# Kernel tuning notes

Measured on AMD Instinct MI355X. Metric: run time of the kernel, lower is better.

Reference implementation:

```python
import jax, jax.numpy as jnp
import numpy as np


def xnorm(x, g):
    # x * gamma / ||x||_2 along last dim (no eps, matching torch.norm)
    n = jnp.sqrt(jnp.sum(x * x, axis=-1, keepdims=True))
    return x * g / n


def setup_inputs() -> dict:
    key = jax.random.key(0)
    ks = jax.random.split(key, 6)
    B, N, D = 8, 8192, 512
    H, DK, DV = 8, 64, 64
    std = 0.001
    return {
        "queries": jax.random.normal(ks[0], (B, N, D), dtype=jnp.float32),
        # weights stored [in, out] (transposed vs torch Linear)
        "Wq": jax.random.normal(ks[1], (D, H * DK), dtype=jnp.float32) * std,
        "bq": jnp.zeros((H * DK,), dtype=jnp.float32),
        "Wk": jax.random.normal(ks[2], (D, H * DK), dtype=jnp.float32) * std,
        "bk": jnp.zeros((H * DK,), dtype=jnp.float32),
        "Wv": jax.random.normal(ks[3], (D, H * DV), dtype=jnp.float32) * std,
        "bv": jnp.zeros((H * DV,), dtype=jnp.float32),
        "Wo": jax.random.normal(ks[4], (H * DV, D), dtype=jnp.float32) * std,
        "bo": jnp.zeros((D,), dtype=jnp.float32),
        "gamma": jax.random.normal(ks[5], (1, H, 1, 1), dtype=jnp.float32),
    }


def reference(queries, Wq, bq, Wk, bk, Wv, bv, Wo, bo, gamma):
    B, N, D = queries.shape
    H, DK = 8, 64
    DV = 64
    q = (queries @ Wq + bq).reshape(B, N, H, DK)  # bnhd
    k = (queries @ Wk + bk).reshape(B, N, H, DK)
    v = (queries @ Wv + bv).reshape(B, N, H, DV)
    # kv = k^T @ v per (batch, head): [B,H,DK,DV]
    kv = jnp.einsum("bnhk,bnhv->bhkv", k, v)
    kv_n = xnorm(kv, gamma)                       # norm over DV axis
    q_n = xnorm(q.transpose(0, 2, 1, 3), gamma)   # bhnd, norm over DK axis
    out = jnp.einsum("bhnk,bhkv->bnhv", q_n, kv_n).reshape(B, N, H * DV)
    return out @ Wo + bo
```

## Files before the change

### kernel.cpp

```cpp
#include <hip/hip_runtime.h>

typedef __attribute__((ext_vector_type(8))) short s8v;
typedef __attribute__((ext_vector_type(4))) float f4v;

__device__ __forceinline__ unsigned short f2bf(float f) {
  unsigned int u = __float_as_uint(f);
  u += 0x7FFFu + ((u >> 16) & 1u);
  return (unsigned short)(u >> 16);
}
__device__ __forceinline__ float bf2f(unsigned short s) {
  return __uint_as_float(((unsigned int)s) << 16);
}

__device__ __forceinline__ void gld16(const void* g, void* l) {
  __builtin_amdgcn_global_load_lds(
      (const __attribute__((address_space(1))) unsigned int*)g,
      (__attribute__((address_space(3))) unsigned int*)l, 16, 0, 0);
}

#define TILE_SYNC() asm volatile("s_waitcnt vmcnt(0) lgkmcnt(0)\n\ts_barrier" ::: "memory")

__global__ __launch_bounds__(256)
void convert_x_kernel(const float* __restrict__ X, unsigned short* __restrict__ Xbf)
{
  size_t base = ((size_t)blockIdx.x * 256 + threadIdx.x) * 8;
  float4 a = *(const float4*)&X[base];
  float4 b = *(const float4*)&X[base + 4];
  s8v p = (s8v){ (short)f2bf(a.x), (short)f2bf(a.y), (short)f2bf(a.z), (short)f2bf(a.w),
                 (short)f2bf(b.x), (short)f2bf(b.y), (short)f2bf(b.z), (short)f2bf(b.w) };
  *(s8v*)&Xbf[base] = p;
}

__global__ __launch_bounds__(256)
void transpose_w_kernel(const float* __restrict__ Wq, const float* __restrict__ Wk,
                        const float* __restrict__ Wv, unsigned short* __restrict__ Wt)
{
  __shared__ float T[64][68];
  const int kt = blockIdx.x, nt = blockIdx.y;
  const float* W = (nt < 8) ? Wq : (nt < 16 ? Wk : Wv);
  const int n0 = (nt & 7) * 64, k0 = kt * 64;
  const int t = threadIdx.x;
  #pragma unroll
  for (int it = 0; it < 4; ++it) {
    int idx = it * 256 + t;
    int k = idx >> 4, n4 = (idx & 15) << 2;
    *(float4*)&T[k][n4] = *(const float4*)&W[(size_t)(k0 + k) * 512 + n0 + n4];
  }
  __syncthreads();
  #pragma unroll
  for (int it = 0; it < 2; ++it) {
    int idx = it * 256 + t;
    int n = idx >> 3, k8 = (idx & 7) << 3;
    s8v p;
    #pragma unroll
    for (int j = 0; j < 8; ++j) p[j] = (short)f2bf(T[k8 + j][n]);
    *(s8v*)&Wt[((size_t)nt * 64 + n) * 512 + k0 + k8] = p;
  }
}

__global__ __launch_bounds__(256, 2)
void gemm_qkv_kernel(const unsigned short* __restrict__ Xbf,
                     const unsigned short* __restrict__ Wt,
                     const float* __restrict__ bq, const float* __restrict__ bk,
                     const float* __restrict__ bv,
                     const float* __restrict__ gamma,
                     unsigned short* __restrict__ qhat,
                     unsigned short* __restrict__ kvT)
{
  __shared__ short As[8192];
  __shared__ short Bs[8192];
  const int t = threadIdx.x;
  const int nb = blockIdx.x, rb = blockIdx.y;
  const int wave = t >> 6, lane = t & 63;
  const int wm = wave & 1, wn = wave >> 1;
  const int quad = lane >> 4, l16 = lane & 15;
  const int row0 = rb * 128;
  const int ncol0 = nb * 128;

  const unsigned short* ap[4];
  const unsigned short* bp[4];
  #pragma unroll
  for (int i = 0; i < 4; ++i) {
    int s = i * 256 + t;
    int m = s >> 3;
    int kb = (s & 7) ^ (m & 7);
    ap[i] = Xbf + (size_t)(row0 + m) * 512 + kb * 8;
    bp[i] = Wt + (size_t)(ncol0 + m) * 512 + kb * 8;
  }

  f4v acc[4][4];
  #pragma unroll
  for (int i = 0; i < 4; ++i)
    #pragma unroll
    for (int j = 0; j < 4; ++j) acc[i][j] = (f4v){0.f, 0.f, 0.f, 0.f};

  for (int kt = 0; kt < 512; kt += 64) {
    __syncthreads();
    #pragma unroll
    for (int i = 0; i < 4; ++i) {
      int s8 = (i * 256 + t) * 8;
      gld16(ap[i] + kt, &As[s8]);
      gld16(bp[i] + kt, &Bs[s8]);
    }
    __syncthreads();
    #pragma unroll
    for (int ks = 0; ks < 2; ++ks) {
      s8v a[4], b[4];
      #pragma unroll
      for (int mi = 0; mi < 4; ++mi) {
        int r = wm * 64 + mi * 16 + l16;
        int slot = r * 8 + ((ks * 4 + quad) ^ (r & 7));
        a[mi] = *(const s8v*)&As[slot * 8];
      }
      #pragma unroll
      for (int nj = 0; nj < 4; ++nj) {
        int r = wn * 64 + nj * 16 + l16;
        int slot = r * 8 + ((ks * 4 + quad) ^ (r & 7));
        b[nj] = *(const s8v*)&Bs[slot * 8];
      }
      #pragma unroll
      for (int mi = 0; mi < 4; ++mi)
        #pragma unroll
        for (int nj = 0; nj < 4; ++nj)
          acc[mi][nj] = __builtin_amdgcn_mfma_f32_16x16x32_bf16(a[mi], b[nj], acc[mi][nj], 0, 0, 0);
    }
  }

  if (nb < 4) {
    #pragma unroll
    for (int nj = 0; nj < 4; ++nj) {
      int colg = ncol0 + wn * 64 + nj * 16 + l16;
      float bias = bq[colg];
      #pragma unroll
      for (int mi = 0; mi < 4; ++mi) {
        acc[mi][nj][0] += bias; acc[mi][nj][1] += bias;
        acc[mi][nj][2] += bias; acc[mi][nj][3] += bias;
      }
    }
    float g = gamma[nb * 2 + wn];
    #pragma unroll
    for (int mi = 0; mi < 4; ++mi)
      #pragma unroll
      for (int rr = 0; rr < 4; ++rr) {
        float ss = acc[mi][0][rr] * acc[mi][0][rr] + acc[mi][1][rr] * acc[mi][1][rr]
                 + acc[mi][2][rr] * acc[mi][2][rr] + acc[mi][3][rr] * acc[mi][3][rr];
        ss += __shfl_xor(ss, 1);
        ss += __shfl_xor(ss, 2);
        ss += __shfl_xor(ss, 4);
        ss += __shfl_xor(ss, 8);
        float scale = g * rsqrtf(ss);
        acc[mi][0][rr] *= scale; acc[mi][1][rr] *= scale;
        acc[mi][2][rr] *= scale; acc[mi][3][rr] *= scale;
      }
    const int colbase = ncol0 + wn * 64;
    #pragma unroll
    for (int mi = 0; mi < 4; ++mi)
      #pragma unroll
      for (int nj = 0; nj < 4; ++nj)
        #pragma unroll
        for (int rr = 0; rr < 4; ++rr) {
          int row = row0 + wm * 64 + mi * 16 + quad * 4 + rr;
          int col = colbase + nj * 16 + l16;
          qhat[(size_t)row * 512 + col] = f2bf(acc[mi][nj][rr]);
        }
  } else {
    const int sect = (nb - 4) >> 2;
    const float* bb = sect ? bv : bk;
    const int bidx = row0 >> 13;
    const int nb4 = (nb - 4) & 3;
    const int nrow = (row0 & 8191) + wm * 64 + quad * 4;
    #pragma unroll
    for (int nj = 0; nj < 4; ++nj) {
      int cis = nb4 * 128 + wn * 64 + nj * 16 + l16;
      float bias = bb[cis];
      int h = cis >> 6, dk = cis & 63;
      unsigned short* rowp = kvT + (size_t)((sect * 64 + bidx * 8 + h) * 64 + dk) * 8192;
      #pragma unroll
      for (int mi = 0; mi < 4; ++mi) {
        unsigned int lo = (unsigned int)f2bf(acc[mi][nj][0] + bias)
                        | ((unsigned int)f2bf(acc[mi][nj][1] + bias) << 16);
        unsigned int hi = (unsigned int)f2bf(acc[mi][nj][2] + bias)
                        | ((unsigned int)f2bf(acc[mi][nj][3] + bias) << 16);
        uint2 pk; pk.x = lo; pk.y = hi;
        *(uint2*)&rowp[nrow + mi * 16] = pk;
      }
    }
  }
}

__global__ __launch_bounds__(256)
void kv_accum_kernel(const unsigned short* __restrict__ kvT, float* __restrict__ kvpart)
{
  const int t = threadIdx.x;
  const int bh = blockIdx.x, chunk = blockIdx.y;
  const int wave = t >> 6, lane = t & 63;
  const int quad = lane >> 4, l16 = lane & 15;
  const unsigned short* kb_ = kvT + (size_t)bh * 64 * 8192;
  const unsigned short* vb_ = kvT + (size_t)(64 + bh) * 64 * 8192;
  const int n0 = chunk * 512 + wave * 128 + quad * 8;

  f4v acc[4][4];
  #pragma unroll
  for (int i = 0; i < 4; ++i)
    #pragma unroll
    for (int j = 0; j < 4; ++j) acc[i][j] = (f4v){0.f, 0.f, 0.f, 0.f};

  s8v a0[4], b0[4], a1[4], b1[4];
  #pragma unroll
  for (int mi = 0; mi < 4; ++mi) {
    a0[mi] = *(const s8v*)&kb_[(size_t)(mi * 16 + l16) * 8192 + n0];
    b0[mi] = *(const s8v*)&vb_[(size_t)(mi * 16 + l16) * 8192 + n0];
  }

#define KV_STEP(AC, BC, AN, BN, S)                                             \
  {                                                                            \
    if ((S) < 3) {                                                             \
      int nn = n0 + ((S) + 1) * 32;                                            \
      _Pragma("unroll")                                                        \
      for (int mi = 0; mi < 4; ++mi) {                                         \
        AN[mi] = *(const s8v*)&kb_[(size_t)(mi * 16 + l16) * 8192 + nn];       \
        BN[mi] = *(const s8v*)&vb_[(size_t)(mi * 16 + l16) * 8192 + nn];       \
      }                                                                        \
    }                                                                          \
    _Pragma("unroll")                                                          \
    for (int mi = 0; mi < 4; ++mi)                                             \
      _Pragma("unroll")                                                        \
      for (int nj = 0; nj < 4; ++nj)                                           \
        acc[mi][nj] = __builtin_amdgcn_mfma_f32_16x16x32_bf16(AC[mi], BC[nj],  \
                                                              acc[mi][nj], 0, 0, 0); \
  }

  KV_STEP(a0, b0, a1, b1, 0)
  KV_STEP(a1, b1, a0, b0, 1)
  KV_STEP(a0, b0, a1, b1, 2)
  KV_STEP(a1, b1, a0, b0, 3)
#undef KV_STEP

  float* dst = kvpart + ((size_t)(chunk * 4 + wave) * 64 + bh) * 4096;
  #pragma unroll
  for (int mi = 0; mi < 4; ++mi)
    #pragma unroll
    for (int nj = 0; nj < 4; ++nj)
      #pragma unroll
      for (int rr = 0; rr < 4; ++rr)
        dst[(mi * 16 + quad * 4 + rr) * 64 + nj * 16 + l16] = acc[mi][nj][rr];
}

__global__ __launch_bounds__(256)
void kv_reduce_kernel(const float* __restrict__ kvpart, float* __restrict__ kvbuf)
{
  const int bh = blockIdx.x, seg = blockIdx.y, t = threadIdx.x;
  #pragma unroll
  for (int e = 0; e < 2; ++e) {
    int i = seg * 512 + e * 256 + t;
    float s = 0.f;
    for (int c = 0; c < 64; ++c) s += kvpart[((size_t)c * 64 + bh) * 4096 + i];
    kvbuf[(size_t)bh * 4096 + i] = s;
  }
}

__global__ __launch_bounds__(256)
void build_w2t_kernel(const float* __restrict__ kvbuf, const float* __restrict__ Wo,
                      const float* __restrict__ gamma, unsigned short* __restrict__ W2t)
{
  __shared__ float WoS[512][16];
  const int b = blockIdx.x, dt = blockIdx.y;
  const int d0 = dt * 16;
  const int t = threadIdx.x;
  for (int i = 0; i < 32; ++i) {
    int flat = i * 256 + t;
    int rr_ = flat >> 4, c = flat & 15;
    WoS[rr_][c] = Wo[(size_t)rr_ * 512 + d0 + c];
  }
  __syncthreads();
  for (int rr = 0; rr < 2; ++rr) {
    int r = rr * 256 + t;
    int h = r >> 6, k = r & 63;
    const float* krow = kvbuf + ((size_t)b * 8 + h) * 4096 + (size_t)k * 64;
    float ss = 0.f;
    #pragma unroll
    for (int v = 0; v < 64; v += 4) {
      float4 x = *(const float4*)&krow[v];
      ss += x.x * x.x + x.y * x.y + x.z * x.z + x.w * x.w;
    }
    float scale = gamma[h] * rsqrtf(ss);
    f4v accv[4];
    #pragma unroll
    for (int j = 0; j < 4; ++j) accv[j] = (f4v){0.f, 0.f, 0.f, 0.f};
    for (int v = 0; v < 64; ++v) {
      float m = krow[v] * scale;
      const float* w = &WoS[h * 64 + v][0];
      #pragma unroll
      for (int j4 = 0; j4 < 4; ++j4) {
        float4 ww = *(const float4*)&w[j4 * 4];
        accv[j4][0] = fmaf(m, ww.x, accv[j4][0]);
        accv[j4][1] = fmaf(m, ww.y, accv[j4][1]);
        accv[j4][2] = fmaf(m, ww.z, accv[j4][2]);
        accv[j4][3] = fmaf(m, ww.w, accv[j4][3]);
      }
    }
    #pragma unroll
    for (int j = 0; j < 16; ++j)
      W2t[((size_t)b * 512 + d0 + j) * 512 + r] = f2bf(accv[j >> 2][j & 3]);
  }
}

__global__ __launch_bounds__(512, 2)
void gemm_out_kernel(const unsigned short* __restrict__ qhat,
                     const unsigned short* __restrict__ W2t,
                     const float* __restrict__ bo,
                     float* __restrict__ out)
{
  __shared__ short As[2][16384];
  __shared__ short Bs[2][16384];
  const int t = threadIdx.x;
  const int o = blockIdx.x;
  const int swz = (o & 7) * 64 + (o >> 3);
  const int nb = swz & 1, rb = swz >> 1;
  const int wave = t >> 6, lane = t & 63;
  const int wm = wave & 1, wn = wave >> 1;
  const int quad = lane >> 4, l16 = lane & 15;
  const int row0 = rb * 256, ncol0 = nb * 256;
  const unsigned short* Wb = W2t + (size_t)(rb >> 5) * 262144;

  const unsigned short* ap[4];
  const unsigned short* bp[4];
  int ldst[4];
  #pragma unroll
  for (int i = 0; i < 4; ++i) {
    int s = i * 512 + t;
    int m = s >> 3, kb = (s & 7) ^ (m & 7);
    ap[i] = qhat + (size_t)(row0 + m) * 512 + kb * 8;
    bp[i] = Wb + (size_t)(ncol0 + m) * 512 + kb * 8;
    ldst[i] = s * 8;
  }

  f4v acc[8][4];
  #pragma unroll
  for (int i = 0; i < 8; ++i)
    #pragma unroll
    for (int j = 0; j < 4; ++j) acc[i][j] = (f4v){0.f, 0.f, 0.f, 0.f};

  #pragma unroll
  for (int i = 0; i < 4; ++i) {
    gld16(ap[i], &As[0][ldst[i]]);
    gld16(bp[i], &Bs[0][ldst[i]]);
  }
  TILE_SYNC();

  for (int kt = 0; kt < 8; ++kt) {
    const int cur = kt & 1;
    const short* Ac = As[cur];
    const short* Bc = Bs[cur];
    short* An = (short*)As[cur ^ 1];
    short* Bn = (short*)Bs[cur ^ 1];
    const int koff = (kt + 1) * 64;
    const bool pf = kt < 7;
    s8v afr[4][2], bfr[4][2];

    if (pf) {
      gld16(ap[0] + koff, &An[ldst[0]]);
      gld16(ap[1] + koff, &An[ldst[1]]);
      gld16(bp[0] + koff, &Bn[ldst[0]]);
      gld16(bp[1] + koff, &Bn[ldst[1]]);
    }
    #pragma unroll
    for (int nj = 0; nj < 4; ++nj)
      #pragma unroll
      for (int ks = 0; ks < 2; ++ks) {
        int r = wn * 64 + nj * 16 + l16;
        bfr[nj][ks] = *(const s8v*)&Bc[(r * 8 + ((ks * 4 + quad) ^ (r & 7))) * 8];
      }
    #pragma unroll
    for (int mi = 0; mi < 4; ++mi)
      #pragma unroll
      for (int ks = 0; ks < 2; ++ks) {
        int r = wm * 128 + mi * 16 + l16;
        afr[mi][ks] = *(const s8v*)&Ac[(r * 8 + ((ks * 4 + quad) ^ (r & 7))) * 8];
      }
    __builtin_amdgcn_s_setprio(1);
    #pragma unroll
    for (int mi = 0; mi < 4; ++mi)
      #pragma unroll
      for (int nj = 0; nj < 2; ++nj)
        #pragma unroll
        for (int ks = 0; ks < 2; ++ks)
          acc[mi][nj] = __builtin_amdgcn_mfma_f32_16x16x32_bf16(afr[mi][ks], bfr[nj][ks], acc[mi][nj], 0, 0, 0);
    __builtin_amdgcn_s_setprio(0);
    __builtin_amdgcn_s_barrier();

    if (pf) {
      gld16(ap[2] + koff, &An[ldst[2]]);
      gld16(ap[3] + koff, &An[ldst[3]]);
      gld16(bp[2] + koff, &Bn[ldst[2]]);
      gld16(bp[3] + koff, &Bn[ldst[3]]);
    }
    __builtin_amdgcn_s_setprio(1);
    #pragma unroll
    for (int mi = 0; mi < 4; ++mi)
      #pragma unroll
      for (int nj = 2; nj < 4; ++nj)
        #pragma unroll
        for (int ks = 0; ks < 2; ++ks)
          acc[mi][nj] = __builtin_amdgcn_mfma_f32_16x16x32_bf16(afr[mi][ks], bfr[nj][ks], acc[mi][nj], 0, 0, 0);
    __builtin_amdgcn_s_setprio(0);
    __builtin_amdgcn_s_barrier();

    #pragma unroll
    for (int mi = 0; mi < 4; ++mi)
      #pragma unroll
      for (int ks = 0; ks < 2; ++ks) {
        int r = wm * 128 + (4 + mi) * 16 + l16;
        afr[mi][ks] = *(const s8v*)&Ac[(r * 8 + ((ks * 4 + quad) ^ (r & 7))) * 8];
      }
    __builtin_amdgcn_s_setprio(1);
    #pragma unroll
    for (int mi = 0; mi < 4; ++mi)
      #pragma unroll
      for (int nj = 0; nj < 2; ++nj)
        #pragma unroll
        for (int ks = 0; ks < 2; ++ks)
          acc[4 + mi][nj] = __builtin_amdgcn_mfma_f32_16x16x32_bf16(afr[mi][ks], bfr[nj][ks], acc[4 + mi][nj], 0, 0, 0);
    __builtin_amdgcn_s_setprio(0);
    __builtin_amdgcn_s_barrier();

    __builtin_amdgcn_s_setprio(1);
    #pragma unroll
    for (int mi = 0; mi < 4; ++mi)
      #pragma unroll
      for (int nj = 2; nj < 4; ++nj)
        #pragma unroll
        for (int ks = 0; ks < 2; ++ks)
          acc[4 + mi][nj] = __builtin_amdgcn_mfma_f32_16x16x32_bf16(afr[mi][ks], bfr[nj][ks], acc[4 + mi][nj], 0, 0, 0);
    __builtin_amdgcn_s_setprio(0);
    TILE_SYNC();
  }

  const int colbase = ncol0 + wn * 64;
  #pragma unroll
  for (int nj = 0; nj < 4; ++nj) {
    float bias = bo[colbase + nj * 16 + l16];
    #pragma unroll
    for (int mi = 0; mi < 8; ++mi)
      #pragma unroll
      for (int rr = 0; rr < 4; ++rr) {
        int row = row0 + wm * 128 + mi * 16 + quad * 4 + rr;
        int col = colbase + nj * 16 + l16;
        out[(size_t)row * 512 + col] = acc[mi][nj][rr] + bias;
      }
  }
}

extern "C" void kernel_launch(void* const* d_in, const int* in_sizes, int n_in,
                              void* d_out, int out_size, void* d_ws, size_t ws_size,
                              hipStream_t stream)
{
  (void)in_sizes; (void)n_in; (void)out_size; (void)ws_size;
  const float* X     = (const float*)d_in[0];
  const float* Wq    = (const float*)d_in[1];
  const float* bq    = (const float*)d_in[2];
  const float* Wk    = (const float*)d_in[3];
  const float* bk    = (const float*)d_in[4];
  const float* Wv    = (const float*)d_in[5];
  const float* bv    = (const float*)d_in[6];
  const float* Wo    = (const float*)d_in[7];
  const float* bo    = (const float*)d_in[8];
  const float* gamma = (const float*)d_in[9];

  char* ws = (char*)d_ws;
  unsigned short* qhat = (unsigned short*)ws;
  unsigned short* kvT  = (unsigned short*)(ws + 67108864);
  unsigned short* Xbf  = (unsigned short*)(ws + 201326592);
  float* kvpart = (float*)(ws + 201326592);
  unsigned short* Wt  = (unsigned short*)(ws + 201326592 + 67108864);
  float* kvbuf        = (float*)(ws + 201326592 + 67108864 + 1572864);
  unsigned short* W2t = (unsigned short*)(ws + 201326592 + 67108864 + 1572864 + 1048576);

  dim3 blk(256);
  convert_x_kernel<<<16384, blk, 0, stream>>>(X, Xbf);
  transpose_w_kernel<<<dim3(8, 24), blk, 0, stream>>>(Wq, Wk, Wv, Wt);
  gemm_qkv_kernel<<<dim3(12, 512), blk, 0, stream>>>(Xbf, Wt, bq, bk, bv, gamma, qhat, kvT);
  kv_accum_kernel<<<dim3(64, 16), blk, 0, stream>>>(kvT, kvpart);
  kv_reduce_kernel<<<dim3(64, 8), blk, 0, stream>>>(kvpart, kvbuf);
  build_w2t_kernel<<<dim3(8, 32), blk, 0, stream>>>(kvbuf, Wo, gamma, W2t);
  gemm_out_kernel<<<512, dim3(512), 0, stream>>>(qhat, W2t, bo, (float*)d_out);
}
```

Before: 504.8 us.

## Retile QKV GEMM to 256x256 double-buffered pipeline with grid swizzle

The QKV projection GEMM moves from 128x128 tiles with 256 threads and single-buffered LDS to 256x256 tiles with 512 threads and double-buffered LDS. Loads for the next k-tile are issued in pieces between MFMA phases, guarded by partial vmcnt waits, and a 1D grid with an XCD-aware swizzle replaces the 2D grid. The output GEMM's pipeline is restructured the same way, dropping intermediate barriers and the full wait at the end of each tile. The aim is to reuse each tile more and hide global-load latency. In exchange, LDS use and register pressure rise (128 KB of LDS per block), which can lower occupancy.

Result: slower. 516.5 us (+2.3%).

```diff
diff --git a/kernel.cpp b/kernel.cpp
--- a/kernel.cpp
+++ b/kernel.cpp
@@ -18,7 +18,11 @@
       (__attribute__((address_space(3))) unsigned int*)l, 16, 0, 0);
 }
 
-#define TILE_SYNC() asm volatile("s_waitcnt vmcnt(0) lgkmcnt(0)\n\ts_barrier" ::: "memory")
+#define WAITVM4() asm volatile("s_waitcnt vmcnt(4)" ::: "memory")
+#define WAITVM2() asm volatile("s_waitcnt vmcnt(2)" ::: "memory")
+#define WAITVM0() asm volatile("s_waitcnt vmcnt(0)" ::: "memory")
+#define WAITLGKM() asm volatile("s_waitcnt lgkmcnt(0)" ::: "memory")
+#define SBAR() asm volatile("s_barrier" ::: "memory")
 
 __global__ __launch_bounds__(256)
 void convert_x_kernel(const float* __restrict__ X, unsigned short* __restrict__ Xbf)
@@ -58,7 +62,7 @@
   }
 }
 
-__global__ __launch_bounds__(256, 2)
+__global__ __launch_bounds__(512, 2)
 void gemm_qkv_kernel(const unsigned short* __restrict__ Xbf,
                      const unsigned short* __restrict__ Wt,
                      const float* __restrict__ bq, const float* __restrict__ bk,
@@ -67,79 +71,132 @@
                      unsigned short* __restrict__ qhat,
                      unsigned short* __restrict__ kvT)
 {
-  __shared__ short As[8192];
-  __shared__ short Bs[8192];
+  __shared__ short As[2][16384];
+  __shared__ short Bs[2][16384];
   const int t = threadIdx.x;
-  const int nb = blockIdx.x, rb = blockIdx.y;
+  const int o = blockIdx.x;
+  const int swz = (o & 7) * 192 + (o >> 3);
+  const int nb = swz % 6, rb = swz / 6;
   const int wave = t >> 6, lane = t & 63;
   const int wm = wave & 1, wn = wave >> 1;
   const int quad = lane >> 4, l16 = lane & 15;
-  const int row0 = rb * 128;
-  const int ncol0 = nb * 128;
+  const int row0 = rb * 256, ncol0 = nb * 256;
 
   const unsigned short* ap[4];
   const unsigned short* bp[4];
+  int ldst[4];
   #pragma unroll
   for (int i = 0; i < 4; ++i) {
-    int s = i * 256 + t;
-    int m = s >> 3;
-    int kb = (s & 7) ^ (m & 7);
+    int s = i * 512 + t;
+    int m = s >> 3, kb = (s & 7) ^ (m & 7);
     ap[i] = Xbf + (size_t)(row0 + m) * 512 + kb * 8;
     bp[i] = Wt + (size_t)(ncol0 + m) * 512 + kb * 8;
-  }
-
-  f4v acc[4][4];
-  #pragma unroll
-  for (int i = 0; i < 4; ++i)
+    ldst[i] = s * 8;
+  }
+
+  f4v acc[8][4];
+  #pragma unroll
+  for (int i = 0; i < 8; ++i)
     #pragma unroll
     for (int j = 0; j < 4; ++j) acc[i][j] = (f4v){0.f, 0.f, 0.f, 0.f};
 
-  for (int kt = 0; kt < 512; kt += 64) {
-    __syncthreads();
-    #pragma unroll
-    for (int i = 0; i < 4; ++i) {
-      int s8 = (i * 256 + t) * 8;
-      gld16(ap[i] + kt, &As[s8]);
-      gld16(bp[i] + kt, &Bs[s8]);
-    }
-    __syncthreads();
-    #pragma unroll
-    for (int ks = 0; ks < 2; ++ks) {
-      s8v a[4], b[4];
-      #pragma unroll
-      for (int mi = 0; mi < 4; ++mi) {
-        int r = wm * 64 + mi * 16 + l16;
-        int slot = r * 8 + ((ks * 4 + quad) ^ (r & 7));
-        a[mi] = *(const s8v*)&As[slot * 8];
-      }
-      #pragma unroll
-      for (int nj = 0; nj < 4; ++nj) {
+  gld16(bp[0], &Bs[0][ldst[0]]);
+  gld16(bp[1], &Bs[0][ldst[1]]);
+  gld16(bp[2], &Bs[0][ldst[2]]);
+  gld16(bp[3], &Bs[0][ldst[3]]);
+  gld16(ap[0], &As[0][ldst[0]]);
+  gld16(ap[2], &As[0][ldst[2]]);
+  gld16(ap[1], &As[0][ldst[1]]);
+  gld16(ap[3], &As[0][ldst[3]]);
+
+  for (int kt = 0; kt < 8; ++kt) {
+    const bool pf = kt < 7;
+    const int cur = kt & 1;
+    const short* Ac = As[cur];
+    const short* Bc = Bs[cur];
+    short* An = (short*)As[cur ^ 1];
+    short* Bn = (short*)Bs[cur ^ 1];
+    const int koff = (kt + 1) * 64;
+    s8v afr[4][2], bfr[4][2];
+
+    if (pf) {
+      gld16(bp[0] + koff, &Bn[ldst[0]]);
+      gld16(bp[1] + koff, &Bn[ldst[1]]);
+    }
+    if (pf) { WAITVM4(); } else { WAITVM2(); }
+    SBAR();
+
+    #pragma unroll
+    for (int nj = 0; nj < 4; ++nj)
+      #pragma unroll
+      for (int ks = 0; ks < 2; ++ks) {
         int r = wn * 64 + nj * 16 + l16;
-        int slot = r * 8 + ((ks * 4 + quad) ^ (r & 7));
-        b[nj] = *(const s8v*)&Bs[slot * 8];
-      }
-      #pragma unroll
-      for (int mi = 0; mi < 4; ++mi)
+        bfr[nj][ks] = *(const s8v*)&Bc[(r * 8 + ((ks * 4 + quad) ^ (r & 7))) * 8];
+      }
+    #pragma unroll
+    for (int mi = 0; mi < 4; ++mi)
+      #pragma unroll
+      for (int ks = 0; ks < 2; ++ks) {
+        int r = wm * 128 + mi * 16 + l16;
+        afr[mi][ks] = *(const s8v*)&Ac[(r * 8 + ((ks * 4 + quad) ^ (r & 7))) * 8];
+      }
+    __builtin_amdgcn_s_setprio(1);
+    #pragma unroll
+    for (int mi = 0; mi < 4; ++mi)
+      #pragma unroll
+      for (int nj = 0; nj < 4; ++nj)
         #pragma unroll
-        for (int nj = 0; nj < 4; ++nj)
-          acc[mi][nj] = __builtin_amdgcn_mfma_f32_16x16x32_bf16(a[mi], b[nj], acc[mi][nj], 0, 0, 0);
-    }
-  }
-
-  if (nb < 4) {
+        for (int ks = 0; ks < 2; ++ks)
+          acc[mi][nj] = __builtin_amdgcn_mfma_f32_16x16x32_bf16(afr[mi][ks], bfr[nj][ks], acc[mi][nj], 0, 0, 0);
+    __builtin_amdgcn_s_setprio(0);
+
+    if (pf) {
+      gld16(bp[2] + koff, &Bn[ldst[2]]);
+      gld16(bp[3] + koff, &Bn[ldst[3]]);
+    }
+    if (pf) { WAITVM4(); } else { WAITVM0(); }
+    SBAR();
+
+    #pragma unroll
+    for (int mi = 0; mi < 4; ++mi)
+      #pragma unroll
+      for (int ks = 0; ks < 2; ++ks) {
+        int r = wm * 128 + 64 + mi * 16 + l16;
+        afr[mi][ks] = *(const s8v*)&Ac[(r * 8 + ((ks * 4 + quad) ^ (r & 7))) * 8];
+      }
+    if (pf) {
+      gld16(ap[0] + koff, &An[ldst[0]]);
+      gld16(ap[2] + koff, &An[ldst[2]]);
+      gld16(ap[1] + koff, &An[ldst[1]]);
+      gld16(ap[3] + koff, &An[ldst[3]]);
+    }
+    __builtin_amdgcn_s_setprio(1);
+    #pragma unroll
+    for (int mi = 0; mi < 4; ++mi)
+      #pragma unroll
+      for (int nj = 0; nj < 4; ++nj)
+        #pragma unroll
+        for (int ks = 0; ks < 2; ++ks)
+          acc[4 + mi][nj] = __builtin_amdgcn_mfma_f32_16x16x32_bf16(afr[mi][ks], bfr[nj][ks], acc[4 + mi][nj], 0, 0, 0);
+    __builtin_amdgcn_s_setprio(0);
+    WAITLGKM();
+    SBAR();
+  }
+
+  if (nb < 2) {
     #pragma unroll
     for (int nj = 0; nj < 4; ++nj) {
       int colg = ncol0 + wn * 64 + nj * 16 + l16;
       float bias = bq[colg];
       #pragma unroll
-      for (int mi = 0; mi < 4; ++mi) {
+      for (int mi = 0; mi < 8; ++mi) {
         acc[mi][nj][0] += bias; acc[mi][nj][1] += bias;
         acc[mi][nj][2] += bias; acc[mi][nj][3] += bias;
       }
     }
-    float g = gamma[nb * 2 + wn];
-    #pragma unroll
-    for (int mi = 0; mi < 4; ++mi)
+    float g = gamma[nb * 4 + wn];
+    #pragma unroll
+    for (int mi = 0; mi < 8; ++mi)
       #pragma unroll
       for (int rr = 0; rr < 4; ++rr) {
         float ss = acc[mi][0][rr] * acc[mi][0][rr] + acc[mi][1][rr] * acc[mi][1][rr]
@@ -154,29 +211,28 @@
       }
     const int colbase = ncol0 + wn * 64;
     #pragma unroll
-    for (int mi = 0; mi < 4; ++mi)
+    for (int mi = 0; mi < 8; ++mi)
       #pragma unroll
       for (int nj = 0; nj < 4; ++nj)
         #pragma unroll
         for (int rr = 0; rr < 4; ++rr) {
-          int row = row0 + wm * 64 + mi * 16 + quad * 4 + rr;
+          int row = row0 + wm * 128 + mi * 16 + quad * 4 + rr;
           int col = colbase + nj * 16 + l16;
           qhat[(size_t)row * 512 + col] = f2bf(acc[mi][nj][rr]);
         }
   } else {
-    const int sect = (nb - 4) >> 2;
+    const int sect = (nb - 2) >> 1;
     const float* bb = sect ? bv : bk;
     const int bidx = row0 >> 13;
-    const int nb4 = (nb - 4) & 3;
-    const int nrow = (row0 & 8191) + wm * 64 + quad * 4;
+    const int nrow = (row0 & 8191) + wm * 128 + quad * 4;
     #pragma unroll
     for (int nj = 0; nj < 4; ++nj) {
-      int cis = nb4 * 128 + wn * 64 + nj * 16 + l16;
+      int cis = ((nb - 2) & 1) * 256 + wn * 64 + nj * 16 + l16;
       float bias = bb[cis];
       int h = cis >> 6, dk = cis & 63;
       unsigned short* rowp = kvT + (size_t)((sect * 64 + bidx * 8 + h) * 64 + dk) * 8192;
       #pragma unroll
-      for (int mi = 0; mi < 4; ++mi) {
+      for (int mi = 0; mi < 8; ++mi) {
         unsigned int lo = (unsigned int)f2bf(acc[mi][nj][0] + bias)
                         | ((unsigned int)f2bf(acc[mi][nj][1] + bias) << 16);
         unsigned int hi = (unsigned int)f2bf(acc[mi][nj][2] + bias)
@@ -341,29 +397,32 @@
     #pragma unroll
     for (int j = 0; j < 4; ++j) acc[i][j] = (f4v){0.f, 0.f, 0.f, 0.f};
 
-  #pragma unroll
-  for (int i = 0; i < 4; ++i) {
-    gld16(ap[i], &As[0][ldst[i]]);
-    gld16(bp[i], &Bs[0][ldst[i]]);
-  }
-  TILE_SYNC();
+  gld16(bp[0], &Bs[0][ldst[0]]);
+  gld16(bp[1], &Bs[0][ldst[1]]);
+  gld16(bp[2], &Bs[0][ldst[2]]);
+  gld16(bp[3], &Bs[0][ldst[3]]);
+  gld16(ap[0], &As[0][ldst[0]]);
+  gld16(ap[2], &As[0][ldst[2]]);
+  gld16(ap[1], &As[0][ldst[1]]);
+  gld16(ap[3], &As[0][ldst[3]]);
 
   for (int kt = 0; kt < 8; ++kt) {
+    const bool pf = kt < 7;
     const int cur = kt & 1;
     const short* Ac = As[cur];
     const short* Bc = Bs[cur];
     short* An = (short*)As[cur ^ 1];
     short* Bn = (short*)Bs[cur ^ 1];
     const int koff = (kt + 1) * 64;
-    const bool pf = kt < 7;
     s8v afr[4][2], bfr[4][2];
 
     if (pf) {
-      gld16(ap[0] + koff, &An[ldst[0]]);
-      gld16(ap[1] + koff, &An[ldst[1]]);
       gld16(bp[0] + koff, &Bn[ldst[0]]);
       gld16(bp[1] + koff, &Bn[ldst[1]]);
     }
+    if (pf) { WAITVM4(); } else { WAITVM2(); }
+    SBAR();
+
     #pragma unroll
     for (int nj = 0; nj < 4; ++nj)
       #pragma unroll
@@ -382,58 +441,43 @@
     #pragma unroll
     for (int mi = 0; mi < 4; ++mi)
       #pragma unroll
-      for (int nj = 0; nj < 2; ++nj)
+      for (int nj = 0; nj < 4; ++nj)
         #pragma unroll
         for (int ks = 0; ks < 2; ++ks)
           acc[mi][nj] = __builtin_amdgcn_mfma_f32_16x16x32_bf16(afr[mi][ks], bfr[nj][ks], acc[mi][nj], 0, 0, 0);
     __builtin_amdgcn_s_setprio(0);
-    __builtin_amdgcn_s_barrier();
 
     if (pf) {
-      gld16(ap[2] + koff, &An[ldst[2]]);
-      gld16(ap[3] + koff, &An[ldst[3]]);
       gld16(bp[2] + koff, &Bn[ldst[2]]);
       gld16(bp[3] + koff, &Bn[ldst[3]]);
     }
+    if (pf) { WAITVM4(); } else { WAITVM0(); }
+    SBAR();
+
+    #pragma unroll
+    for (int mi = 0; mi < 4; ++mi)
+      #pragma unroll
+      for (int ks = 0; ks < 2; ++ks) {
+        int r = wm * 128 + 64 + mi * 16 + l16;
+        afr[mi][ks] = *(const s8v*)&Ac[(r * 8 + ((ks * 4 + quad) ^ (r & 7))) * 8];
+      }
+    if (pf) {
+      gld16(ap[0] + koff, &An[ldst[0]]);
+      gld16(ap[2] + koff, &An[ldst[2]]);
+      gld16(ap[1] + koff, &An[ldst[1]]);
+      gld16(ap[3] + koff, &An[ldst[3]]);
+    }
     __builtin_amdgcn_s_setprio(1);
     #pragma unroll
     for (int mi = 0; mi < 4; ++mi)
       #pragma unroll
-      for (int nj = 2; nj < 4; ++nj)
-        #pragma unroll
-        for (int ks = 0; ks < 2; ++ks)
-          acc[mi][nj] = __builtin_amdgcn_mfma_f32_16x16x32_bf16(afr[mi][ks], bfr[nj][ks], acc[mi][nj], 0, 0, 0);
-    __builtin_amdgcn_s_setprio(0);
-    __builtin_amdgcn_s_barrier();
-
-    #pragma unroll
-    for (int mi = 0; mi < 4; ++mi)
-      #pragma unroll
-      for (int ks = 0; ks < 2; ++ks) {
-        int r = wm * 128 + (4 + mi) * 16 + l16;
-        afr[mi][ks] = *(const s8v*)&Ac[(r * 8 + ((ks * 4 + quad) ^ (r & 7))) * 8];
-      }
-    __builtin_amdgcn_s_setprio(1);
-    #pragma unroll
-    for (int mi = 0; mi < 4; ++mi)
-      #pragma unroll
-      for (int nj = 0; nj < 2; ++nj)
+      for (int nj = 0; nj < 4; ++nj)
         #pragma unroll
         for (int ks = 0; ks < 2; ++ks)
           acc[4 + mi][nj] = __builtin_amdgcn_mfma_f32_16x16x32_bf16(afr[mi][ks], bfr[nj][ks], acc[4 + mi][nj], 0, 0, 0);
     __builtin_amdgcn_s_setprio(0);
-    __builtin_amdgcn_s_barrier();
-
-    __builtin_amdgcn_s_setprio(1);
-    #pragma unroll
-    for (int mi = 0; mi < 4; ++mi)
-      #pragma unroll
-      for (int nj = 2; nj < 4; ++nj)
-        #pragma unroll
-        for (int ks = 0; ks < 2; ++ks)
-          acc[4 + mi][nj] = __builtin_amdgcn_mfma_f32_16x16x32_bf16(afr[mi][ks], bfr[nj][ks], acc[4 + mi][nj], 0, 0, 0);
-    __builtin_amdgcn_s_setprio(0);
-    TILE_SYNC();
+    WAITLGKM();
+    SBAR();
   }
 
   const int colbase = ncol0 + wn * 64;
@@ -479,7 +523,7 @@
   dim3 blk(256);
   convert_x_kernel<<<16384, blk, 0, stream>>>(X, Xbf);
   transpose_w_kernel<<<dim3(8, 24), blk, 0, stream>>>(Wq, Wk, Wv, Wt);
-  gemm_qkv_kernel<<<dim3(12, 512), blk, 0, stream>>>(Xbf, Wt, bq, bk, bv, gamma, qhat, kvT);
+  gemm_qkv_kernel<<<1536, dim3(512), 0, stream>>>(Xbf, Wt, bq, bk, bv, gamma, qhat, kvT);
   kv_accum_kernel<<<dim3(64, 16), blk, 0, stream>>>(kvT, kvpart);
   kv_reduce_kernel<<<dim3(64, 8), blk, 0, stream>>>(kvpart, kvbuf);
   build_w2t_kernel<<<dim3(8, 32), blk, 0, stream>>>(kvbuf, Wo, gamma, W2t);
```

## Stage K/V transposed stores through LDS and swizzle QKV GEMM block order

Applied to the files above, without the earlier changes.

The K/V epilogue of the QKV GEMM now writes its bf16 tile into shared memory with an XOR swizzle, then reads it back so each wave writes 128-byte contiguous row segments of the transposed kvT buffer. Before, each lane issued scattered 8-byte stores. The grid is also flattened to 1D and remapped so consecutive blocks are spread across XCD-style groups of 8, which changes which blocks run together and may improve L2 reuse of the X and W tiles. The cost is two extra barriers and an LDS round trip in the epilogue.

New measurement: 500.9 us. No clear change (-0.8%).

```diff
diff --git a/kernel.cpp b/kernel.cpp
--- a/kernel.cpp
+++ b/kernel.cpp
@@ -70,7 +70,9 @@
   __shared__ short As[8192];
   __shared__ short Bs[8192];
   const int t = threadIdx.x;
-  const int nb = blockIdx.x, rb = blockIdx.y;
+  const int o = blockIdx.x;
+  const int swz = (o & 7) * 768 + (o >> 3);
+  const int nb = swz % 12, rb = swz / 12;
   const int wave = t >> 6, lane = t & 63;
   const int wm = wave & 1, wn = wave >> 1;
   const int quad = lane >> 4, l16 = lane & 15;
@@ -167,23 +169,36 @@
     const int sect = (nb - 4) >> 2;
     const float* bb = sect ? bv : bk;
     const int bidx = row0 >> 13;
-    const int nb4 = (nb - 4) & 3;
-    const int nrow = (row0 & 8191) + wm * 64 + quad * 4;
+    const int cis0 = ((nb - 4) & 3) * 128 + wn * 64;
+    const int h = cis0 >> 6;
+    short* base = (wave < 2) ? &As[wave * 4096] : &Bs[(wave - 2) * 4096];
+    __syncthreads();
     #pragma unroll
     for (int nj = 0; nj < 4; ++nj) {
-      int cis = nb4 * 128 + wn * 64 + nj * 16 + l16;
-      float bias = bb[cis];
-      int h = cis >> 6, dk = cis & 63;
-      unsigned short* rowp = kvT + (size_t)((sect * 64 + bidx * 8 + h) * 64 + dk) * 8192;
+      int ld = nj * 16 + l16;
+      float bias = bb[cis0 + ld];
+      int c = (ld & 15) << 2;
       #pragma unroll
       for (int mi = 0; mi < 4; ++mi) {
+        int ln4 = mi * 16 + quad * 4;
         unsigned int lo = (unsigned int)f2bf(acc[mi][nj][0] + bias)
                         | ((unsigned int)f2bf(acc[mi][nj][1] + bias) << 16);
         unsigned int hi = (unsigned int)f2bf(acc[mi][nj][2] + bias)
                         | ((unsigned int)f2bf(acc[mi][nj][3] + bias) << 16);
         uint2 pk; pk.x = lo; pk.y = hi;
-        *(uint2*)&rowp[nrow + mi * 16] = pk;
-      }
+        *(uint2*)&base[ld * 64 + (ln4 ^ c)] = pk;
+      }
+    }
+    __syncthreads();
+    const int nbase = (row0 & 8191) + wm * 64;
+    unsigned short* secp = kvT + (size_t)((sect * 64 + bidx * 8 + h) * 64) * 8192;
+    #pragma unroll
+    for (int pass = 0; pass < 16; ++pass) {
+      int rowd = pass * 4 + (lane >> 4);
+      int ng = (lane & 15) * 4;
+      int c2 = (rowd & 15) << 2;
+      uint2 v = *(const uint2*)&base[rowd * 64 + (ng ^ c2)];
+      *(uint2*)&secp[(size_t)rowd * 8192 + nbase + ng] = v;
     }
   }
 }
@@ -479,7 +494,7 @@
   dim3 blk(256);
   convert_x_kernel<<<16384, blk, 0, stream>>>(X, Xbf);
   transpose_w_kernel<<<dim3(8, 24), blk, 0, stream>>>(Wq, Wk, Wv, Wt);
-  gemm_qkv_kernel<<<dim3(12, 512), blk, 0, stream>>>(Xbf, Wt, bq, bk, bv, gamma, qhat, kvT);
+  gemm_qkv_kernel<<<6144, blk, 0, stream>>>(Xbf, Wt, bq, bk, bv, gamma, qhat, kvT);
   kv_accum_kernel<<<dim3(64, 16), blk, 0, stream>>>(kvT, kvpart);
   kv_reduce_kernel<<<dim3(64, 8), blk, 0, stream>>>(kvpart, kvbuf);
   build_w2t_kernel<<<dim3(8, 32), blk, 0, stream>>>(kvbuf, Wo, gamma, W2t);
```
